# Performance work log

Measured on AMD Instinct MI355X. Metric: run time of the kernel, lower is better.

## Reference

```python
import jax, jax.numpy as jnp
import numpy as np

E, DEPTH, H, T_BLOCK, VOC = 1024, 8, 16, 2048, 256
DH = E // H
B, T = 4, 2048
EPS = 1e-5


def _layernorm(x, g, b):
    mu = jnp.mean(x, axis=-1, keepdims=True)
    var = jnp.mean(jnp.square(x - mu), axis=-1, keepdims=True)
    return (x - mu) * jax.lax.rsqrt(var + EPS) * g + b


def setup_inputs() -> dict:
    key = jax.random.key(0)
    ks = iter(jax.random.split(key, 32))

    def xav(k, shape):
        fan_in, fan_out = shape[-2], shape[-1]
        lim = np.sqrt(6.0 / (fan_in + fan_out))
        return jax.random.uniform(k, shape, jnp.float32, -lim, lim)

    inp = {
        "tokens": jax.random.randint(next(ks), (B, T), 0, VOC),
        "emb_w": xav(next(ks), (VOC, E)),
        "pos_w": xav(next(ks), (T_BLOCK, E)),
        # per-layer stacked params
        "Wq": xav(next(ks), (DEPTH, H, E, DH)),
        "Wk": xav(next(ks), (DEPTH, H, E, DH)),
        "Wv": xav(next(ks), (DEPTH, H, E, DH)),
        "Wo": xav(next(ks), (DEPTH, E, E)),        # stored [in, out]
        "ln1_g": jnp.ones((DEPTH, E)), "ln1_b": jnp.zeros((DEPTH, E)),
        "W1": xav(next(ks), (DEPTH, E, 4 * E)), "b1": jnp.zeros((DEPTH, 4 * E)),
        "W2": xav(next(ks), (DEPTH, 4 * E, E)), "b2": jnp.zeros((DEPTH, E)),
        "ln2_g": jnp.ones((DEPTH, E)), "ln2_b": jnp.zeros((DEPTH, E)),
        "lnf_g": jnp.ones((E,)), "lnf_b": jnp.zeros((E,)),
        "Wu": xav(next(ks), (E, 2)), "bu": jnp.zeros((2,)),
    }
    return inp


def _forward(tokens, emb_w, pos_w, Wq, Wk, Wv, Wo, ln1_g, ln1_b,
             W1, b1, W2, b2, ln2_g, ln2_b, lnf_g, lnf_b, Wu, bu):
    Tlen = tokens.shape[1]
    x = emb_w[tokens] + pos_w[:Tlen]                       # [B, T, E]
    scale = 1.0 / jnp.sqrt(jnp.float32(Tlen))              # NOTE: original divides by sqrt(seq_len)
    for l in range(Wq.shape[0]):
        h = _layernorm(x, ln1_g[l], ln1_b[l])
        q = jnp.einsum('hed,bte->bhtd', Wq[l], h)
        k = jnp.einsum('hed,bte->bhtd', Wk[l], h)
        v = jnp.einsum('hed,bte->bhtd', Wv[l], h)
        scores = jnp.einsum('bhtd,bhsd->bhts', q, k) * scale
        attn = jax.nn.softmax(scores, axis=-1)
        att = jnp.einsum('bhts,bhsd->bhtd', attn, v)       # [B, H, T, DH]
        att = att.transpose(0, 2, 1, 3).reshape(x.shape)   # b t (h d)
        x = x + att @ Wo[l]
        h = _layernorm(x, ln2_g[l], ln2_b[l])
        x = x + jax.nn.relu(h @ W1[l] + b1[l]) @ W2[l] + b2[l]
    x = _layernorm(x, lnf_g, lnf_b)
    return x @ Wu + bu                                     # [B, T, 2]


def reference(tokens, emb_w, pos_w, Wq, Wk, Wv, Wo, ln1_g, ln1_b,
              W1, b1, W2, b2, ln2_g, ln2_b, lnf_g, lnf_b, Wu, bu):
    return _forward(tokens, emb_w, pos_w, Wq, Wk, Wv, Wo, ln1_g, ln1_b,
                    W1, b1, W2, b2, ln2_g, ln2_b, lnf_g, lnf_b, Wu, bu)
```

## Files before the change

kernel.cpp:

```cpp
#include <hip/hip_runtime.h>
#include <hip/hip_bf16.h>
#include <math.h>

#define E_DIM 1024
#define T_SEQ 2048
#define NH 16
#define DHEAD 64
#define NB 4
#define NLAYER 8

typedef __attribute__((ext_vector_type(8))) short bf16x8;
typedef __attribute__((ext_vector_type(4))) short short4v;
typedef __attribute__((ext_vector_type(4))) float f32x4;

#if __has_builtin(__builtin_amdgcn_exp2f)
#define EXP2(x) __builtin_amdgcn_exp2f(x)
#else
#define EXP2(x) exp2f(x)
#endif

static __device__ __forceinline__ short f2bf(float f) {
  union { __hip_bfloat16 h; short s; } u;
  u.h = __float2bfloat16(f);
  return u.s;
}
static __device__ __forceinline__ float bf2f(short s) {
  union { unsigned u; float f; } v;
  v.u = ((unsigned)(unsigned short)s) << 16;
  return v.f;
}

static __device__ __forceinline__ void gload16(const short* g, short* l) {
  __builtin_amdgcn_global_load_lds(
      (const __attribute__((address_space(1))) unsigned*)(g),
      (__attribute__((address_space(3))) unsigned*)(l), 16, 0, 0);
}

static __device__ __forceinline__ int xcd_swz(int orig, int nwg) {
  return (orig & 7) * (nwg >> 3) + (orig >> 3);
}

__global__ __launch_bounds__(256) void embed_kernel(const int* __restrict__ tokens,
    const float* __restrict__ emb, const float* __restrict__ pos, float* __restrict__ x) {
  int idx = blockIdx.x * 256 + threadIdx.x;
  int bt = idx >> 10;
  int e  = idx & 1023;
  int t  = bt & (T_SEQ - 1);
  int tok = tokens[bt];
  x[idx] = emb[tok * E_DIM + e] + pos[t * E_DIM + e];
}

__global__ __launch_bounds__(256) void ln_bf16_kernel(const float* __restrict__ x,
    const float* __restrict__ g, const float* __restrict__ b, short* __restrict__ out) {
  __shared__ float s1[4], s2[4];
  int row = blockIdx.x;
  const float4* xr = (const float4*)(x + (size_t)row * E_DIM);
  float4 xv = xr[threadIdx.x];
  float s = xv.x + xv.y + xv.z + xv.w;
  float q = xv.x*xv.x + xv.y*xv.y + xv.z*xv.z + xv.w*xv.w;
  #pragma unroll
  for (int off = 32; off; off >>= 1) {
    s += __shfl_xor(s, off, 64);
    q += __shfl_xor(q, off, 64);
  }
  int lane = threadIdx.x & 63, wid = threadIdx.x >> 6;
  if (lane == 0) { s1[wid] = s; s2[wid] = q; }
  __syncthreads();
  float mean = (s1[0] + s1[1] + s1[2] + s1[3]) * (1.0f / E_DIM);
  float ms   = (s2[0] + s2[1] + s2[2] + s2[3]) * (1.0f / E_DIM);
  float rstd = rsqrtf(ms - mean * mean + 1e-5f);
  float4 gv = ((const float4*)g)[threadIdx.x];
  float4 bv = ((const float4*)b)[threadIdx.x];
  short4v ov;
  ov.x = f2bf((xv.x - mean) * rstd * gv.x + bv.x);
  ov.y = f2bf((xv.y - mean) * rstd * gv.y + bv.y);
  ov.z = f2bf((xv.z - mean) * rstd * gv.z + bv.z);
  ov.w = f2bf((xv.w - mean) * rstd * gv.w + bv.w);
  *(short4v*)(out + (size_t)row * E_DIM + threadIdx.x * 4) = ov;
}

struct PrepP {
  const float *s0, *s1, *s2, *s3, *s4, *s5;
  short *d0, *d1, *d2, *d3, *d4, *d5;
};

__global__ void prep_kernel(PrepP p) {
  __shared__ float tile[32][33];
  int bid = blockIdx.x;
  const float* src; short* dst; int K, N, kb, local;
  if (bid < 1024)      { src = p.s0; dst = p.d0; K = 1024; N = 64;   kb = 32;  local = bid; }
  else if (bid < 2048) { src = p.s1; dst = p.d1; K = 1024; N = 64;   kb = 32;  local = bid - 1024; }
  else if (bid < 3072) { src = p.s2; dst = p.d2; K = 1024; N = 64;   kb = 32;  local = bid - 2048; }
  else if (bid < 4096) { src = p.s3; dst = p.d3; K = 1024; N = 1024; kb = 32;  local = bid - 3072; }
  else if (bid < 8192) { src = p.s4; dst = p.d4; K = 1024; N = 4096; kb = 32;  local = bid - 4096; }
  else                 { src = p.s5; dst = p.d5; K = 4096; N = 1024; kb = 128; local = bid - 8192; }
  int per = kb * (N >> 5);
  int z = local / per, rem = local % per;
  int k0 = (rem % kb) * 32, n0 = (rem / kb) * 32;
  src += (size_t)z * K * N;
  dst += (size_t)z * N * K;
  int tx = threadIdx.x, ty = threadIdx.y;
  #pragma unroll
  for (int i = 0; i < 4; ++i)
    tile[ty + 8 * i][tx] = src[(size_t)(k0 + ty + 8 * i) * N + n0 + tx];
  __syncthreads();
  #pragma unroll
  for (int i = 0; i < 4; ++i)
    dst[(size_t)(n0 + ty + 8 * i) * K + k0 + tx] = f2bf(tile[tx][ty + 8 * i]);
}

struct GemmP {
  const short* A; const short* B; void* C;
  const float* bias; const float* res;
  long sAb, sAt, sAh;
  long sBh, sBd;
  long sCb, sCt, sCh;
  int K; float alpha; int alphaN; int gridx;
  int relu; int cbf16; int hasbias; int hasres;
};

__global__ __launch_bounds__(256, 2) void gemm_bf16(GemmP p) {
  __shared__ __align__(16) short As[2][128 * 64];
  __shared__ __align__(16) short Bs[2][128 * 64];
  const int t = threadIdx.x;
  const int lane = t & 63, wid = t >> 6;
  const int wr = wid >> 1, wc = wid & 1;
  const int wg = xcd_swz(blockIdx.x, gridDim.x);
  const long bm = (long)(wg / p.gridx) * 128, bn = (long)(wg % p.gridx) * 128;

  const int srow8 = lane >> 3;
  const int schunk = (lane & 7) ^ srow8;
  const short* aS[4]; const short* bS[4];
  #pragma unroll
  for (int i = 0; i < 4; ++i) {
    long m = bm + i * 32 + wid * 8 + srow8;
    long n = bn + i * 32 + wid * 8 + srow8;
    aS[i] = p.A + (m >> 11) * p.sAb + (m & 2047) * p.sAt + schunk * 8;
    bS[i] = p.B + (n >> 6) * p.sBh + (n & 63) * p.sBd + schunk * 8;
  }

  const int rA = lane & 15, g = lane >> 4;
  f32x4 acc[4][4] = {};
  const int NT = p.K >> 6;

  #pragma unroll
  for (int i = 0; i < 4; ++i) { gload16(aS[i], &As[0][i * 2048 + wid * 512]); aS[i] += p.sAh; }
  #pragma unroll
  for (int i = 0; i < 4; ++i) { gload16(bS[i], &Bs[0][i * 2048 + wid * 512]); bS[i] += 64; }
  asm volatile("s_waitcnt vmcnt(0)" ::: "memory");
  __builtin_amdgcn_s_barrier();

  int cur = 0;
  for (int kt = 0; kt < NT; ++kt) {
    const int ns = cur ^ 1;
    if (kt + 1 < NT) {
      #pragma unroll
      for (int i = 0; i < 4; ++i) { gload16(aS[i], &As[ns][i * 2048 + wid * 512]); aS[i] += p.sAh; }
      #pragma unroll
      for (int i = 0; i < 4; ++i) { gload16(bS[i], &Bs[ns][i * 2048 + wid * 512]); bS[i] += 64; }
    }
    bf16x8 af[4][2], bf[4][2];
    #pragma unroll
    for (int kk = 0; kk < 2; ++kk) {
      const int ch = ((g + kk * 4) ^ (rA & 7)) * 8;
      #pragma unroll
      for (int f = 0; f < 4; ++f) {
        af[f][kk] = *(const bf16x8*)&As[cur][(wr * 64 + f * 16 + rA) * 64 + ch];
        bf[f][kk] = *(const bf16x8*)&Bs[cur][(wc * 64 + f * 16 + rA) * 64 + ch];
      }
    }
    asm volatile("s_waitcnt lgkmcnt(0)" ::: "memory");
    __builtin_amdgcn_sched_barrier(0);
    __builtin_amdgcn_s_setprio(1);
    #pragma unroll
    for (int kk = 0; kk < 2; ++kk)
      #pragma unroll
      for (int i = 0; i < 4; ++i)
        #pragma unroll
        for (int j = 0; j < 4; ++j)
          acc[i][j] = __builtin_amdgcn_mfma_f32_16x16x32_bf16(af[i][kk], bf[j][kk], acc[i][j], 0, 0, 0);
    __builtin_amdgcn_s_setprio(0);
    if (kt + 1 < NT) {
      asm volatile("s_waitcnt vmcnt(0)" ::: "memory");
      __builtin_amdgcn_s_barrier();
    }
    cur = ns;
  }

  float bias4[4], aa4[4];
  long ncol[4];
  #pragma unroll
  for (int j = 0; j < 4; ++j) {
    long n = bn + wc * 64 + j * 16 + rA;
    ncol[j] = (n >> 6) * p.sCh + (n & 63);
    bias4[j] = p.hasbias ? p.bias[n] : 0.f;
    aa4[j] = (n < p.alphaN) ? p.alpha : 1.0f;
  }
  #pragma unroll
  for (int i = 0; i < 4; ++i) {
    #pragma unroll
    for (int r = 0; r < 4; ++r) {
      long m = bm + wr * 64 + i * 16 + g * 4 + r;
      long mb = (m >> 11) * p.sCb + (m & 2047) * p.sCt;
      #pragma unroll
      for (int j = 0; j < 4; ++j) {
        long ca = mb + ncol[j];
        float v = aa4[j] * acc[i][j][r] + bias4[j];
        if (p.relu) v = fmaxf(v, 0.f);
        if (p.hasres) v += p.res[ca];
        if (p.cbf16) ((short*)p.C)[ca] = f2bf(v);
        else ((float*)p.C)[ca] = v;
      }
    }
  }
}

__global__ __launch_bounds__(512) void attn_mfma_kernel(const short* __restrict__ qkv,
                                                        short* __restrict__ att) {
  __shared__ __align__(16) short Ks[64 * 64];
  __shared__ __align__(16) short Vt[64 * 64];
  __shared__ __align__(16) short Pq[8 * 16 * 64];

  const int t = threadIdx.x;
  const int lane = t & 63, wid = t >> 6;
  const int wg = xcd_swz(blockIdx.x, gridDim.x);
  const int bh = wg >> 4;
  const int b = bh >> 4, h = bh & 15;
  const int q0blk = (wg & 15) * 128;
  const int rA = lane & 15;
  const int g  = lane >> 4;
  const int xq = (rA & 7) << 3;
  const float L2E = 1.4426950408889634f;

  const short* Qg = qkv + (size_t)b * 6291456 + (size_t)h * 131072;
  const short* Kg = Qg + 2097152;
  const short* Vg = Qg + 4194304;

  const int q0w = q0blk + wid * 16;
  bf16x8 qf0 = *(const bf16x8*)(Qg + (size_t)(q0w + rA) * DHEAD + g * 8);
  bf16x8 qf1 = *(const bf16x8*)(Qg + (size_t)(q0w + rA) * DHEAD + 32 + g * 8);

  bf16x8 ones;
  #pragma unroll
  for (int j = 0; j < 8; ++j) ones[j] = (short)0x3F80;

  short* Pw = Pq + wid * 1024;
  const int ss = t >> 3, sp = t & 7;

  float mrun = -1e30f;
  f32x4 lrun4 = {};
  f32x4 acco[4] = {};

  bf16x8 kreg = *(const bf16x8*)(Kg + (size_t)ss * DHEAD + sp * 8);
  bf16x8 vreg = *(const bf16x8*)(Vg + (size_t)ss * DHEAD + sp * 8);

  for (int tile = 0; tile < T_SEQ / 64; ++tile) {
    __syncthreads();
    *(bf16x8*)&Ks[ss * 64 + ((sp ^ (ss & 7)) << 3)] = kreg;
    #pragma unroll
    for (int j = 0; j < 8; ++j) {
      int d = sp * 8 + j;
      Vt[d * 64 + ((ss + 8 * (sp + j)) & 63)] = vreg[j];
    }
    __syncthreads();
    if (tile + 1 < T_SEQ / 64) {
      kreg = *(const bf16x8*)(Kg + (size_t)((tile + 1) * 64 + ss) * DHEAD + sp * 8);
      vreg = *(const bf16x8*)(Vg + (size_t)((tile + 1) * 64 + ss) * DHEAD + sp * 8);
    }

    f32x4 accs[4];
    __builtin_amdgcn_s_setprio(1);
    #pragma unroll
    for (int st = 0; st < 4; ++st) {
      int srow = st * 16 + rA;
      bf16x8 kf0 = *(const bf16x8*)&Ks[srow * 64 + ((g ^ (rA & 7)) << 3)];
      bf16x8 kf1 = *(const bf16x8*)&Ks[srow * 64 + (((g + 4) ^ (rA & 7)) << 3)];
      f32x4 z = {};
      z = __builtin_amdgcn_mfma_f32_16x16x32_bf16(kf0, qf0, z, 0, 0, 0);
      accs[st] = __builtin_amdgcn_mfma_f32_16x16x32_bf16(kf1, qf1, z, 0, 0, 0);
    }
    __builtin_amdgcn_s_setprio(0);

    float tm = fmaxf(accs[0][0], accs[0][1]);
    tm = fmaxf(tm, fmaxf(accs[0][2], accs[0][3]));
    #pragma unroll
    for (int st = 1; st < 4; ++st) {
      tm = fmaxf(tm, fmaxf(accs[st][0], accs[st][1]));
      tm = fmaxf(tm, fmaxf(accs[st][2], accs[st][3]));
    }

    float pv[16];
    if (__all(tm - mrun <= 8.0f)) {
      float mL = mrun * L2E;
      #pragma unroll
      for (int st = 0; st < 4; ++st)
        #pragma unroll
        for (int r = 0; r < 4; ++r)
          pv[st * 4 + r] = EXP2(fmaf(accs[st][r], L2E, -mL));
    } else {
      float tmr = fmaxf(tm, __shfl_xor(tm, 16));
      tmr = fmaxf(tmr, __shfl_xor(tmr, 32));
      float mnew = fmaxf(mrun, tmr);
      float mL = mnew * L2E;
      float corr = EXP2((mrun - mnew) * L2E);
      mrun = mnew;
      #pragma unroll
      for (int st = 0; st < 4; ++st)
        #pragma unroll
        for (int r = 0; r < 4; ++r)
          pv[st * 4 + r] = EXP2(fmaf(accs[st][r], L2E, -mL));
      float c4r[4];
      #pragma unroll
      for (int r = 0; r < 4; ++r) c4r[r] = __shfl(corr, g * 4 + r);
      #pragma unroll
      for (int r = 0; r < 4; ++r) lrun4[r] *= c4r[r];
      #pragma unroll
      for (int dt = 0; dt < 4; ++dt)
        #pragma unroll
        for (int r = 0; r < 4; ++r) acco[dt][r] *= c4r[r];
    }

    #pragma unroll
    for (int st = 0; st < 4; ++st) {
      short4v pk;
      pk.x = f2bf(pv[st * 4 + 0]);
      pk.y = f2bf(pv[st * 4 + 1]);
      pk.z = f2bf(pv[st * 4 + 2]);
      pk.w = f2bf(pv[st * 4 + 3]);
      *(short4v*)&Pw[(rA * 64 + st * 16 + g * 4) ^ xq] = pk;
    }
    asm volatile("s_waitcnt lgkmcnt(0)" ::: "memory");

    __builtin_amdgcn_s_setprio(1);
    #pragma unroll
    for (int sk = 0; sk < 2; ++sk) {
      bf16x8 pf = *(const bf16x8*)&Pw[(rA * 64 + sk * 32 + g * 8) ^ xq];
      lrun4 = __builtin_amdgcn_mfma_f32_16x16x32_bf16(pf, ones, lrun4, 0, 0, 0);
      #pragma unroll
      for (int dt = 0; dt < 4; ++dt) {
        int d = dt * 16 + rA;
        bf16x8 vf = *(const bf16x8*)&Vt[d * 64 +
            ((sk * 32 + g * 8 + 8 * (dt * 2 + (rA >> 3) + (rA & 7))) & 63)];
        acco[dt] = __builtin_amdgcn_mfma_f32_16x16x32_bf16(pf, vf, acco[dt], 0, 0, 0);
      }
    }
    __builtin_amdgcn_s_setprio(0);
  }

  float l4[4];
  #pragma unroll
  for (int r = 0; r < 4; ++r) l4[r] = 1.0f / lrun4[r];
  #pragma unroll
  for (int dt = 0; dt < 4; ++dt)
    #pragma unroll
    for (int r = 0; r < 4; ++r)
      att[(size_t)bh * T_SEQ * DHEAD + (size_t)(q0w + g * 4 + r) * DHEAD + dt * 16 + rA] =
          f2bf(acco[dt][r] * l4[r]);
}

__global__ __launch_bounds__(256) void head_kernel(const short* __restrict__ h,
    const float* __restrict__ Wu, const float* __restrict__ bu, float* __restrict__ out) {
  __shared__ float sm[8];
  int row = blockIdx.x;
  const short* hr = h + (size_t)row * E_DIM;
  float a0 = 0.f, a1 = 0.f;
  for (int i = threadIdx.x; i < E_DIM; i += 256) {
    float hv = bf2f(hr[i]);
    a0 = fmaf(hv, Wu[i * 2 + 0], a0);
    a1 = fmaf(hv, Wu[i * 2 + 1], a1);
  }
  #pragma unroll
  for (int off = 32; off; off >>= 1) {
    a0 += __shfl_xor(a0, off, 64);
    a1 += __shfl_xor(a1, off, 64);
  }
  int lane = threadIdx.x & 63, wid = threadIdx.x >> 6;
  if (lane == 0) { sm[wid] = a0; sm[4 + wid] = a1; }
  __syncthreads();
  if (threadIdx.x == 0) {
    out[row * 2 + 0] = sm[0] + sm[1] + sm[2] + sm[3] + bu[0];
    out[row * 2 + 1] = sm[4] + sm[5] + sm[6] + sm[7] + bu[1];
  }
}

static inline void launch_gemm(hipStream_t stream, int N,
    const short* A, long sAb, long sAt, long sAh,
    const short* B, long sBh, long sBd,
    void* C, long sCb, long sCt, long sCh,
    const float* bias, const float* res, int K, float alpha, int alphaN,
    int relu, int cbf16) {
  GemmP p;
  p.A = A; p.B = B; p.C = C; p.bias = bias; p.res = res;
  p.sAb = sAb; p.sAt = sAt; p.sAh = sAh;
  p.sBh = sBh; p.sBd = sBd;
  p.sCb = sCb; p.sCt = sCt; p.sCh = sCh;
  p.K = K; p.alpha = alpha; p.alphaN = alphaN; p.gridx = N / 128;
  p.relu = relu; p.cbf16 = cbf16;
  p.hasbias = bias != nullptr; p.hasres = res != nullptr;
  int nwg = (N / 128) * ((NB * T_SEQ) / 128);
  gemm_bf16<<<nwg, 256, 0, stream>>>(p);
}

extern "C" void kernel_launch(void* const* d_in, const int* in_sizes, int n_in,
                              void* d_out, int out_size, void* d_ws, size_t ws_size,
                              hipStream_t stream) {
  const int*   tokens = (const int*)d_in[0];
  const float* emb_w  = (const float*)d_in[1];
  const float* pos_w  = (const float*)d_in[2];
  const float* Wq     = (const float*)d_in[3];
  const float* Wk     = (const float*)d_in[4];
  const float* Wv     = (const float*)d_in[5];
  const float* Wo     = (const float*)d_in[6];
  const float* ln1_g  = (const float*)d_in[7];
  const float* ln1_b  = (const float*)d_in[8];
  const float* W1     = (const float*)d_in[9];
  const float* b1     = (const float*)d_in[10];
  const float* W2     = (const float*)d_in[11];
  const float* b2     = (const float*)d_in[12];
  const float* ln2_g  = (const float*)d_in[13];
  const float* ln2_b  = (const float*)d_in[14];
  const float* lnf_g  = (const float*)d_in[15];
  const float* lnf_b  = (const float*)d_in[16];
  const float* Wu     = (const float*)d_in[17];
  const float* bu     = (const float*)d_in[18];
  float* out = (float*)d_out;

  char* ws = (char*)d_ws;
  float* X     = (float*)(ws);
  short* Hb    = (short*)(ws + 33554432);
  short* QKVb  = (short*)(ws + 50331648);
  short* FFH   = (short*)(ws + 100663296);
  short* WqkvT = (short*)(ws + 167772160);
  short* WoT   = (short*)(ws + 174063616);
  short* W1T   = (short*)(ws + 176160768);
  short* W2T   = (short*)(ws + 184549376);

  const float scale = 0.022097086912079608f;

  embed_kernel<<<32768, 256, 0, stream>>>(tokens, emb_w, pos_w, X);

  for (int l = 0; l < NLAYER; ++l) {
    PrepP pp;
    pp.s0 = Wq + (size_t)l * 1048576; pp.d0 = WqkvT;
    pp.s1 = Wk + (size_t)l * 1048576; pp.d1 = WqkvT + 1048576;
    pp.s2 = Wv + (size_t)l * 1048576; pp.d2 = WqkvT + 2097152;
    pp.s3 = Wo + (size_t)l * 1048576; pp.d3 = WoT;
    pp.s4 = W1 + (size_t)l * 4194304; pp.d4 = W1T;
    pp.s5 = W2 + (size_t)l * 4194304; pp.d5 = W2T;
    prep_kernel<<<12288, dim3(32, 8), 0, stream>>>(pp);

    ln_bf16_kernel<<<8192, 256, 0, stream>>>(X, ln1_g + l * 1024, ln1_b + l * 1024, Hb);

    launch_gemm(stream, 3072, Hb, 2097152, 1024, 64, WqkvT, 65536, 1024,
                QKVb, 6291456, 64, 131072, nullptr, nullptr, 1024, scale, 1024, 0, 1);

    attn_mfma_kernel<<<1024, 512, 0, stream>>>(QKVb, Hb);

    launch_gemm(stream, 1024, Hb, 2097152, 64, 131072, WoT, 65536, 1024,
                X, 2097152, 1024, 64, nullptr, X, 1024, 1.0f, 0, 0, 0);

    ln_bf16_kernel<<<8192, 256, 0, stream>>>(X, ln2_g + l * 1024, ln2_b + l * 1024, Hb);

    launch_gemm(stream, 4096, Hb, 2097152, 1024, 64, W1T, 65536, 1024,
                FFH, 8388608, 4096, 64, b1 + (size_t)l * 4096, nullptr, 1024, 1.0f, 0, 1, 1);
    launch_gemm(stream, 1024, FFH, 8388608, 4096, 64, W2T, 262144, 4096,
                X, 2097152, 1024, 64, b2 + (size_t)l * 1024, X, 4096, 1.0f, 0, 0, 0);
  }

  ln_bf16_kernel<<<8192, 256, 0, stream>>>(X, lnf_g, lnf_b, Hb);
  head_kernel<<<8192, 256, 0, stream>>>(Hb, Wu, bu, out);
}
```

Baseline: 3.347 ms.

## Widen GEMM tile to 128x256 with 512 threads and triple-buffered LDS

The GEMM block grows from 128x128 with 4 waves to 128x256 with 8 waves, so each A tile is reused across twice as many output columns. The LDS pipeline moves from double to triple buffering, with loads issued two k-steps ahead and partial vmcnt waits, to hide more global latency. This uses 144KB of dynamic LDS and one block per CU, which reduces occupancy and halves the number of workgroups. That fewer workgroups may hurt load balance on the wave-count-limited grids.

```diff
diff --git a/kernel.cpp b/kernel.cpp
--- a/kernel.cpp
+++ b/kernel.cpp
@@ -119,54 +119,63 @@
   int relu; int cbf16; int hasbias; int hasres;
 };
 
-__global__ __launch_bounds__(256, 2) void gemm_bf16(GemmP p) {
-  __shared__ __align__(16) short As[2][128 * 64];
-  __shared__ __align__(16) short Bs[2][128 * 64];
+__global__ __launch_bounds__(512, 1) void gemm_bf16(GemmP p) {
+  extern __shared__ __align__(16) short Lsh[];
+  constexpr int ASZ  = 128 * 64;
+  constexpr int SLOT = ASZ + 256 * 64;
+
   const int t = threadIdx.x;
   const int lane = t & 63, wid = t >> 6;
-  const int wr = wid >> 1, wc = wid & 1;
+  const int wm = wid >> 2, wn = wid & 3;
+  const int rA = lane & 15, g = lane >> 4;
   const int wg = xcd_swz(blockIdx.x, gridDim.x);
-  const long bm = (long)(wg / p.gridx) * 128, bn = (long)(wg % p.gridx) * 128;
+  const long bm = (long)(wg / p.gridx) * 128, bn = (long)(wg % p.gridx) * 256;
 
   const int srow8 = lane >> 3;
   const int schunk = (lane & 7) ^ srow8;
-  const short* aS[4]; const short* bS[4];
+  const short* aS[2]; const short* bS[4];
+  #pragma unroll
+  for (int i = 0; i < 2; ++i) {
+    long m = bm + i * 64 + wid * 8 + srow8;
+    aS[i] = p.A + (m >> 11) * p.sAb + (m & 2047) * p.sAt + schunk * 8;
+  }
   #pragma unroll
   for (int i = 0; i < 4; ++i) {
-    long m = bm + i * 32 + wid * 8 + srow8;
-    long n = bn + i * 32 + wid * 8 + srow8;
-    aS[i] = p.A + (m >> 11) * p.sAb + (m & 2047) * p.sAt + schunk * 8;
+    long n = bn + i * 64 + wid * 8 + srow8;
     bS[i] = p.B + (n >> 6) * p.sBh + (n & 63) * p.sBd + schunk * 8;
   }
-
-  const int rA = lane & 15, g = lane >> 4;
+  const int dOff = wid * 512;
+
+#define ISSUE_TILE(slot)                                                      \
+  {                                                                           \
+    short* sb = Lsh + (slot) * SLOT;                                          \
+    _Pragma("unroll")                                                         \
+    for (int i = 0; i < 2; ++i) { gload16(aS[i], sb + i * 4096 + dOff); aS[i] += p.sAh; } \
+    _Pragma("unroll")                                                         \
+    for (int i = 0; i < 4; ++i) { gload16(bS[i], sb + ASZ + i * 4096 + dOff); bS[i] += 64; } \
+  }
+
   f32x4 acc[4][4] = {};
   const int NT = p.K >> 6;
 
-  #pragma unroll
-  for (int i = 0; i < 4; ++i) { gload16(aS[i], &As[0][i * 2048 + wid * 512]); aS[i] += p.sAh; }
-  #pragma unroll
-  for (int i = 0; i < 4; ++i) { gload16(bS[i], &Bs[0][i * 2048 + wid * 512]); bS[i] += 64; }
-  asm volatile("s_waitcnt vmcnt(0)" ::: "memory");
+  ISSUE_TILE(0)
+  ISSUE_TILE(1)
+  asm volatile("s_waitcnt vmcnt(6)" ::: "memory");
   __builtin_amdgcn_s_barrier();
 
-  int cur = 0;
+  int rd = 0;
   for (int kt = 0; kt < NT; ++kt) {
-    const int ns = cur ^ 1;
-    if (kt + 1 < NT) {
-      #pragma unroll
-      for (int i = 0; i < 4; ++i) { gload16(aS[i], &As[ns][i * 2048 + wid * 512]); aS[i] += p.sAh; }
-      #pragma unroll
-      for (int i = 0; i < 4; ++i) { gload16(bS[i], &Bs[ns][i * 2048 + wid * 512]); bS[i] += 64; }
-    }
+    const int wr2 = rd + 2 >= 3 ? rd - 1 : rd + 2;
+    if (kt + 2 < NT) ISSUE_TILE(wr2)
+    const short* sb = Lsh + rd * SLOT;
     bf16x8 af[4][2], bf[4][2];
     #pragma unroll
     for (int kk = 0; kk < 2; ++kk) {
       const int ch = ((g + kk * 4) ^ (rA & 7)) * 8;
       #pragma unroll
       for (int f = 0; f < 4; ++f) {
-        af[f][kk] = *(const bf16x8*)&As[cur][(wr * 64 + f * 16 + rA) * 64 + ch];
-        bf[f][kk] = *(const bf16x8*)&Bs[cur][(wc * 64 + f * 16 + rA) * 64 + ch];
+        af[f][kk] = *(const bf16x8*)&sb[(wm * 64 + f * 16 + rA) * 64 + ch];
+        bf[f][kk] = *(const bf16x8*)&sb[ASZ + (wn * 64 + f * 16 + rA) * 64 + ch];
       }
     }
     asm volatile("s_waitcnt lgkmcnt(0)" ::: "memory");
@@ -181,17 +190,19 @@
           acc[i][j] = __builtin_amdgcn_mfma_f32_16x16x32_bf16(af[i][kk], bf[j][kk], acc[i][j], 0, 0, 0);
     __builtin_amdgcn_s_setprio(0);
     if (kt + 1 < NT) {
-      asm volatile("s_waitcnt vmcnt(0)" ::: "memory");
+      if (kt + 2 < NT) { asm volatile("s_waitcnt vmcnt(6)" ::: "memory"); }
+      else             { asm volatile("s_waitcnt vmcnt(0)" ::: "memory"); }
       __builtin_amdgcn_s_barrier();
     }
-    cur = ns;
-  }
+    rd = rd + 1 >= 3 ? 0 : rd + 1;
+  }
+#undef ISSUE_TILE
 
   float bias4[4], aa4[4];
   long ncol[4];
   #pragma unroll
   for (int j = 0; j < 4; ++j) {
-    long n = bn + wc * 64 + j * 16 + rA;
+    long n = bn + wn * 64 + j * 16 + rA;
     ncol[j] = (n >> 6) * p.sCh + (n & 63);
     bias4[j] = p.hasbias ? p.bias[n] : 0.f;
     aa4[j] = (n < p.alphaN) ? p.alpha : 1.0f;
@@ -200,7 +211,7 @@
   for (int i = 0; i < 4; ++i) {
     #pragma unroll
     for (int r = 0; r < 4; ++r) {
-      long m = bm + wr * 64 + i * 16 + g * 4 + r;
+      long m = bm + wm * 64 + i * 16 + g * 4 + r;
       long mb = (m >> 11) * p.sCb + (m & 2047) * p.sCt;
       #pragma unroll
       for (int j = 0; j < 4; ++j) {
@@ -394,11 +405,11 @@
   p.sAb = sAb; p.sAt = sAt; p.sAh = sAh;
   p.sBh = sBh; p.sBd = sBd;
   p.sCb = sCb; p.sCt = sCt; p.sCh = sCh;
-  p.K = K; p.alpha = alpha; p.alphaN = alphaN; p.gridx = N / 128;
+  p.K = K; p.alpha = alpha; p.alphaN = alphaN; p.gridx = N / 256;
   p.relu = relu; p.cbf16 = cbf16;
   p.hasbias = bias != nullptr; p.hasres = res != nullptr;
-  int nwg = (N / 128) * ((NB * T_SEQ) / 128);
-  gemm_bf16<<<nwg, 256, 0, stream>>>(p);
+  int nwg = (N / 256) * ((NB * T_SEQ) / 128);
+  gemm_bf16<<<nwg, 512, 147456, stream>>>(p);
 }
 
 extern "C" void kernel_launch(void* const* d_in, const int* in_sizes, int n_in,
```

After: 3.198 ms. 1.05x faster.
